# Performance work log

Measured on AMD Instinct MI355X. Metric: run time of the kernel, lower is better.

Reference implementation:

```python
import jax, jax.numpy as jnp
import numpy as np

D_MODEL = 512
STATE = 128
HALF = STATE // 2
SEQ = 4096
BATCH = 8


def setup_inputs() -> dict:
    key = jax.random.key(0)
    ks = jax.random.split(key, 4)
    u = jax.random.normal(ks[0], (BATCH, SEQ, D_MODEL), dtype=jnp.float32)
    # HiPPO init: Lambda = -0.5 + i*pi*n, n=1..HALF
    n = jnp.arange(1, HALF + 1, dtype=jnp.float32)
    log_Lambda_real = jnp.log(jnp.full((HALF,), 0.5, dtype=jnp.float32))  # log(-real) with real=-0.5
    Lambda_imag = jnp.pi * n
    B_real = jnp.ones((HALF, D_MODEL), dtype=jnp.float32)
    B_imag = jnp.zeros((HALF, D_MODEL), dtype=jnp.float32)
    C_real = jax.random.normal(ks[1], (D_MODEL, HALF), dtype=jnp.float32) / np.sqrt(STATE)
    C_imag = jax.random.normal(ks[2], (D_MODEL, HALF), dtype=jnp.float32) / np.sqrt(STATE)
    D = jax.random.normal(ks[3], (D_MODEL, D_MODEL), dtype=jnp.float32) / np.sqrt(D_MODEL)
    log_Delta = jnp.array([-3.0], dtype=jnp.float32)
    return {
        "u": u,
        "log_Lambda_real": log_Lambda_real,
        "Lambda_imag": Lambda_imag,
        "B_real": B_real,
        "B_imag": B_imag,
        "C_real": C_real,
        "C_imag": C_imag,
        "D": D,
        "log_Delta": log_Delta,
    }


def reference(u, log_Lambda_real, Lambda_imag, B_real, B_imag, C_real, C_imag, D, log_Delta):
    T = u.shape[1]
    Bc = B_real + 1j * B_imag            # (N/2, P) complex
    Cc = C_real + 1j * C_imag            # (P, N/2) complex
    # --- bilinear (Tustin) discretization ---
    Delta = jnp.exp(log_Delta)           # (1,)
    Lambda = -jnp.exp(jnp.clip(log_Lambda_real, -10.0, 10.0)) + 1j * Lambda_imag  # (N/2,)
    denom = 1.0 - (Delta / 2.0) * Lambda
    A_bar = (1.0 + (Delta / 2.0) * Lambda) / denom          # (N/2,)
    B_bar = (Delta / denom)[:, None] * Bc                   # (N/2, P)
    # --- FFT convolution with the SSM kernel k[n,t] = A_bar[n]^t ---
    t_idx = jnp.arange(T)
    k = jnp.exp(jnp.log(A_bar)[:, None] * t_idx[None, :])   # (N/2, T)
    u_c = u.astype(jnp.complex64)
    v = jnp.einsum('np,btp->bnt', B_bar, u_c)               # (B, N/2, T)
    fft_size = 2 * T
    V_f = jnp.fft.fft(v, n=fft_size, axis=-1)
    K_f = jnp.fft.fft(k, n=fft_size, axis=-1)
    conv = jnp.fft.ifft(V_f * K_f[None, :, :], axis=-1)[..., :T]  # (B, N/2, T)
    y = 2.0 * jnp.einsum('pn,bnt->btp', Cc, conv).real      # (B, T, P)
    return y + u @ D.T
```

## Files before the change

kernel.cpp:

```cpp
#include <hip/hip_runtime.h>
#include <hip/hip_bf16.h>
#include <stdint.h>


#define BATCH 8
#define SEQ   4096
#define DMODEL 512
#define HALF  64
#define CHUNK 64
#define NCHUNK (SEQ / CHUNK)
#define NT    10

typedef __attribute__((ext_vector_type(8))) short short8;
typedef __attribute__((ext_vector_type(4))) float f32x4;

__device__ __forceinline__ unsigned short f2bf(float f) {
    unsigned int u = __float_as_uint(f);
    u += 0x7fffu + ((u >> 16) & 1u);
    return (unsigned short)(u >> 16);
}
__device__ __forceinline__ float bf2f(unsigned short s) {
    return __uint_as_float((unsigned)s << 16);
}

__device__ __forceinline__ void poleA(const float* logLr, const float* Li_in,
                                      const float* logDelta, int n,
                                      float& Ar, float& Ai) {
    float Delta = expf(logDelta[0]);
    float llr = fminf(fmaxf(logLr[n], -10.f), 10.f);
    float Lr = -expf(llr);
    float Li = Li_in[n];
    float dr = 1.f - 0.5f * Delta * Lr;
    float di = -0.5f * Delta * Li;
    float dn = dr * dr + di * di;
    float nr = 1.f + 0.5f * Delta * Lr;
    float ni = 0.5f * Delta * Li;
    Ar = (nr * dr + ni * di) / dn;
    Ai = (ni * dr - nr * di) / dn;
}

__device__ __forceinline__ void cpow(float Ar, float Ai, int e,
                                     float& wr, float& wi) {
    wr = 1.f; wi = 0.f;
    float br = Ar, bi = Ai;
#pragma unroll
    for (int k = 0; k < 6; ++k) {
        if (e & 1) { float t = wr * br - wi * bi; wi = wr * bi + wi * br; wr = t; }
        float t2 = br * br - bi * bi; bi = 2.f * br * bi; br = t2;
        e >>= 1;
    }
}

#define GLOAD_LDS16(g, l)                                                    \
    __builtin_amdgcn_global_load_lds(                                        \
        (const __attribute__((address_space(1))) unsigned int*)(g),          \
        (__attribute__((address_space(3))) unsigned int*)(l), 16, 0, 0)

__global__ void k_build(const float* __restrict__ logLr, const float* __restrict__ Li_in,
                        const float* __restrict__ logDelta,
                        const float* __restrict__ Br, const float* __restrict__ Bi,
                        const float* __restrict__ Cr, const float* __restrict__ Ci,
                        const float* __restrict__ D,
                        unsigned short* __restrict__ Mv, unsigned short* __restrict__ W) {
    int bid = blockIdx.x;
    if (bid < 128) {
        int np = bid, p = threadIdx.x;
        if (p < DMODEL) {
            int n = np & 63;
            float Delta = expf(logDelta[0]);
            float llr = fminf(fmaxf(logLr[n], -10.f), 10.f);
            float Lr = -expf(llr);
            float Li = Li_in[n];
            float dr = 1.f - 0.5f * Delta * Lr;
            float di = -0.5f * Delta * Li;
            float dn = dr * dr + di * di;
            float sr = Delta * dr / dn;
            float si = -Delta * di / dn;
            float br = Br[n * DMODEL + p], bi = Bi[n * DMODEL + p];
            float v = (np < HALF) ? (sr * br - si * bi) : (si * br + sr * bi);
            Mv[np * DMODEL + p] = f2bf(v);
        }
    } else {
        int p = bid - 128, j = threadIdx.x;
        float v;
        if (j < HALF) v = 2.f * Cr[p * HALF + j];
        else if (j < 2 * HALF) v = -2.f * Ci[p * HALF + (j - HALF)];
        else v = D[p * DMODEL + (j - 2 * HALF)];
        W[p * 640 + j] = f2bf(v);
    }
}

__global__ void k_scanCB(const unsigned short* __restrict__ Vb,
                         const float* __restrict__ E,
                         const float* __restrict__ logLr, const float* __restrict__ Li_in,
                         const float* __restrict__ logDelta,
                         unsigned short* __restrict__ Xb) {
    int tid = threadIdx.x;
    int n = tid & 63;
    int c = ((blockIdx.x & 31) << 1) + (tid >> 6);
    int b = blockIdx.x >> 5;
    float Ar, Ai;
    poleA(logLr, Li_in, logDelta, n, Ar, Ai);
    float a64r = Ar, a64i = Ai;
#pragma unroll
    for (int s = 0; s < 6; ++s) {
        float t = a64r * a64r - a64i * a64i;
        a64i = 2.f * a64r * a64i;
        a64r = t;
    }
    float xr = 0.f, xi = 0.f, wr = 1.f, wi = 0.f;
    for (int jj = 1; jj <= c; ++jj) {
        int ei = ((b * NCHUNK + (c - jj)) * 2) * HALF + n;
        float er = E[ei], ev = E[ei + 64];
        xr += wr * er - wi * ev;
        xi += wr * ev + wi * er;
        float nwr = wr * a64r - wi * a64i;
        float nwi = wr * a64i + wi * a64r;
        wr = nwr; wi = nwi;
    }
    size_t base = ((size_t)b * SEQ + (size_t)c * CHUNK) * 128 + n;
    for (int tl = 0; tl < CHUNK; ++tl) {
        float vr = bf2f(Vb[base]), vi = bf2f(Vb[base + 64]);
        float nxr = Ar * xr - Ai * xi + vr;
        float nxi = Ar * xi + Ai * xr + vi;
        xr = nxr; xi = nxi;
        Xb[base] = f2bf(xr); Xb[base + 64] = f2bf(xi);
        base += 128;
    }
}

__global__ __launch_bounds__(512) void gemm1(const float* __restrict__ U,
                                             const unsigned short* __restrict__ Mv,
                                             unsigned short* __restrict__ Vb,
                                             unsigned short* __restrict__ Ub,
                                             const float* __restrict__ logLr,
                                             const float* __restrict__ Li_in,
                                             const float* __restrict__ logDelta,
                                             float* __restrict__ E) {
    __shared__ __align__(16) unsigned short As[64 * 32];
    __shared__ __align__(16) unsigned short Bs[128 * 32];
    __shared__ float Ered[8][2][16][2];
    const int tid = threadIdx.x;
    const int lane = tid & 63;
    const int w = tid >> 6;
    const int wm = w >> 2, wn = w & 3;
    const int l15 = lane & 15, l4 = lane >> 4;
    const int row0 = blockIdx.x * 64;
    const int srow = tid >> 3;
    const int sh = (tid & 7) * 4;

    f32x4 acc[2][2];
#pragma unroll
    for (int m = 0; m < 2; ++m)
#pragma unroll
        for (int n = 0; n < 2; ++n) acc[m][n] = (f32x4)(0.f);

    for (int k0 = 0; k0 < DMODEL; k0 += 32) {
        const float4 av = *(const float4*)(U + (size_t)(row0 + srow) * DMODEL + k0 + sh);

        __syncthreads();

        GLOAD_LDS16(Mv + (size_t)(tid >> 2) * DMODEL + k0 + (tid & 3) * 8,
                    &Bs[(w * 64) * 8]);

        uint2 wa;
        wa.x = (unsigned)f2bf(av.x) | ((unsigned)f2bf(av.y) << 16);
        wa.y = (unsigned)f2bf(av.z) | ((unsigned)f2bf(av.w) << 16);
        *(uint2*)&As[srow * 32 + sh] = wa;
        *(uint2*)&Ub[(size_t)(row0 + srow) * DMODEL + k0 + sh] = wa;

        __syncthreads();

        short8 af[2], bf[2];
#pragma unroll
        for (int m = 0; m < 2; ++m)
            af[m] = *(const short8*)&As[(wm * 32 + m * 16 + l15) * 32 + l4 * 8];
#pragma unroll
        for (int n = 0; n < 2; ++n)
            bf[n] = *(const short8*)&Bs[(wn * 32 + n * 16 + l15) * 32 + l4 * 8];
#pragma unroll
        for (int m = 0; m < 2; ++m)
#pragma unroll
            for (int n = 0; n < 2; ++n)
                acc[m][n] = __builtin_amdgcn_mfma_f32_16x16x32_bf16(af[m], bf[n], acc[m][n], 0, 0, 0);
    }

#pragma unroll
    for (int m = 0; m < 2; ++m) {
        int rbase = row0 + wm * 32 + m * 16 + l4 * 4;
#pragma unroll
        for (int n = 0; n < 2; ++n) {
            int col = wn * 32 + n * 16 + l15;
#pragma unroll
            for (int r = 0; r < 4; ++r)
                Vb[(size_t)(rbase + r) * 128 + col] = f2bf(acc[m][n][r]);
        }
    }

    {
        const int base = wm * 32 + l4 * 4;
        const int isIm = (wn >= 2);
#pragma unroll
        for (int nf = 0; nf < 2; ++nf) {
            int pole = ((wn & 1) * 32) + nf * 16 + l15;
            float Ar, Ai;
            poleA(logLr, Li_in, logDelta, pole, Ar, Ai);
            float a2r = Ar * Ar - Ai * Ai, a2i = 2.f * Ar * Ai;
            float a4r = a2r * a2r - a2i * a2i, a4i = 2.f * a2r * a2i;
            float a8r = a4r * a4r - a4i * a4i, a8i = 2.f * a4r * a4i;
            float a12r = a8r * a4r - a8i * a4i, a12i = a8r * a4i + a8i * a4r;
            float wr, wi;
            cpow(Ar, Ai, 44 - base, wr, wi);
            float s2re = 0.f, s2im = 0.f;
#pragma unroll
            for (int m = 1; m >= 0; --m) {
#pragma unroll
                for (int r = 3; r >= 0; --r) {
                    float v = acc[m][nf][r];
                    if (isIm) { s2re -= wi * v; s2im += wr * v; }
                    else      { s2re += wr * v; s2im += wi * v; }
                    float nwr = wr * Ar - wi * Ai;
                    float nwi = wr * Ai + wi * Ar;
                    wr = nwr; wi = nwi;
                }
                if (m == 1) {
                    float nwr = wr * a12r - wi * a12i;
                    float nwi = wr * a12i + wi * a12r;
                    wr = nwr; wi = nwi;
                }
            }
            s2re += __shfl_xor(s2re, 16, 64);
            s2re += __shfl_xor(s2re, 32, 64);
            s2im += __shfl_xor(s2im, 16, 64);
            s2im += __shfl_xor(s2im, 32, 64);
            if (l4 == 0) {
                Ered[w][nf][l15][0] = s2re;
                Ered[w][nf][l15][1] = s2im;
            }
        }
    }
    __syncthreads();
    if (tid < 128) {
        int p = tid & 63;
        int comp = tid >> 6;
        int wn1 = p >> 5;
        int nf = (p >> 4) & 1;
        int l = p & 15;
        float s = Ered[0 * 4 + wn1][nf][l][comp] + Ered[0 * 4 + wn1 + 2][nf][l][comp]
                + Ered[1 * 4 + wn1][nf][l][comp] + Ered[1 * 4 + wn1 + 2][nf][l][comp];
        int b = row0 >> 12;
        int c = (row0 >> 6) & 63;
        E[((b * NCHUNK + c) * 2) * HALF + comp * 64 + p] = s;
    }
}


#define STAGE_K(t, kh, j) do {                                                 \
    int c_ = (kh) * 1024 + (j) * 512 + tid;                                    \
    int ct_ = c_ ^ (((c_ >> 5) & 1) << 1);                                     \
    int r_ = (ct_ >> 2) & 255;                                                 \
    int kcol_ = (t) * 64 + (kh) * 32 + (ct_ & 3) * 8;                          \
    const unsigned short* asrc_ = (kcol_ < 128)                                \
        ? Xb + (size_t)(row0 + r_) * 128 + kcol_                               \
        : Ub + (size_t)(row0 + r_) * 512 + (kcol_ - 128);                      \
    GLOAD_LDS16(asrc_, &As[((t) & 1) * 16384 + ((kh) * 1024 + (j) * 512 + w * 64) * 8]); \
    GLOAD_LDS16(W + (size_t)(col0 + r_) * 640 + kcol_,                         \
                &Bs[((t) & 1) * 16384 + ((kh) * 1024 + (j) * 512 + w * 64) * 8]); \
} while (0)

#define LDAB(t, kh) do {                                                       \
    _Pragma("unroll") for (int i_ = 0; i_ < 8; ++i_) {                         \
        int r_ = wm * 128 + i_ * 16 + l15;                                     \
        int c_ = (l4 * 8) ^ (((r_ >> 3) & 1) << 4);                            \
        af[i_] = *(const short8*)&As[((t) & 1) * 16384 + (kh) * 8192 + r_ * 32 + c_]; \
    }                                                                          \
    _Pragma("unroll") for (int j_ = 0; j_ < 4; ++j_) {                         \
        int r_ = wn * 64 + j_ * 16 + l15;                                      \
        int c_ = (l4 * 8) ^ (((r_ >> 3) & 1) << 4);                            \
        bf[j_] = *(const short8*)&Bs[((t) & 1) * 16384 + (kh) * 8192 + r_ * 32 + c_]; \
    } } while (0)

#define MFMA32() do {                                                          \
    __builtin_amdgcn_s_setprio(1);                                             \
    _Pragma("unroll") for (int i_ = 0; i_ < 8; ++i_)                           \
    _Pragma("unroll") for (int j_ = 0; j_ < 4; ++j_)                           \
        acc[i_][j_] = __builtin_amdgcn_mfma_f32_16x16x32_bf16(                 \
            bf[j_], af[i_], acc[i_][j_], 0, 0, 0);                             \
    __builtin_amdgcn_s_setprio(0);                                             \
} while (0)

#define PHASE_SYNC(N) do {                                                     \
    asm volatile("s_waitcnt vmcnt(" #N ")" ::: "memory");                      \
    __builtin_amdgcn_s_barrier();                                              \
    __builtin_amdgcn_sched_barrier(0);                                         \
} while (0)

__global__ __launch_bounds__(512) void gemm23_8p(const unsigned short* __restrict__ Xb,
                                                 const unsigned short* __restrict__ Ub,
                                                 const unsigned short* __restrict__ W,
                                                 float* __restrict__ C) {
    __shared__ __align__(16) unsigned short As[2 * 16384];
    __shared__ __align__(16) unsigned short Bs[2 * 16384];
    const int tid = threadIdx.x;
    const int lane = tid & 63;
    const int w = tid >> 6;
    const int wm = w >> 2, wn = w & 3;
    const int l15 = lane & 15, l4 = lane >> 4;

    int lin = blockIdx.y * gridDim.x + blockIdx.x;
    int sw = (lin & 7) * 32 + (lin >> 3);
    const int row0 = (sw & 127) * 256;
    const int col0 = (sw >> 7) * 256;

    f32x4 acc[8][4];
#pragma unroll
    for (int m = 0; m < 8; ++m)
#pragma unroll
        for (int n = 0; n < 4; ++n) acc[m][n] = (f32x4)(0.f);

    STAGE_K(0, 0, 0); STAGE_K(0, 0, 1);
    STAGE_K(0, 1, 0); STAGE_K(0, 1, 1);
    STAGE_K(1, 0, 0); STAGE_K(1, 0, 1);

    short8 af[8], bf[4];
    for (int t = 0; t < NT - 1; ++t) {
        PHASE_SYNC(8);
        LDAB(t, 0);
        STAGE_K(t + 1, 1, 0); STAGE_K(t + 1, 1, 1);
        MFMA32();
        PHASE_SYNC(8);
        LDAB(t, 1);
        if (t < NT - 2) { STAGE_K(t + 2, 0, 0); STAGE_K(t + 2, 0, 1); }
        MFMA32();
    }
    PHASE_SYNC(4);
    LDAB(NT - 1, 0);
    MFMA32();
    PHASE_SYNC(0);
    LDAB(NT - 1, 1);
    MFMA32();

#pragma unroll
    for (int i = 0; i < 8; ++i) {
        int row = row0 + wm * 128 + i * 16 + l15;
#pragma unroll
        for (int j = 0; j < 4; ++j) {
            int col = col0 + wn * 64 + j * 16 + l4 * 4;
            *(float4*)&C[(size_t)row * DMODEL + col] =
                make_float4(acc[i][j][0], acc[i][j][1], acc[i][j][2], acc[i][j][3]);
        }
    }
}


extern "C" void kernel_launch(void* const* d_in, const int* in_sizes, int n_in,
                              void* d_out, int out_size, void* d_ws, size_t ws_size,
                              hipStream_t stream) {
    const float* u      = (const float*)d_in[0];
    const float* logLr  = (const float*)d_in[1];
    const float* Li     = (const float*)d_in[2];
    const float* Br     = (const float*)d_in[3];
    const float* Bi     = (const float*)d_in[4];
    const float* Cr     = (const float*)d_in[5];
    const float* Ci     = (const float*)d_in[6];
    const float* D      = (const float*)d_in[7];
    const float* logDel = (const float*)d_in[8];
    float* out = (float*)d_out;

    const size_t M = (size_t)BATCH * SEQ;
    unsigned short* Vb = (unsigned short*)d_ws;
    unsigned short* Ub = Vb + M * 128;
    unsigned short* Xb = Ub + M * 512;
    unsigned short* Mv = Xb + M * 128;
    unsigned short* W  = Mv + 128 * 512;
    float* E     = (float*)(W + 512 * 640);

    hipLaunchKernelGGL(k_build, dim3(640), dim3(640), 0, stream,
                       logLr, Li, logDel, Br, Bi, Cr, Ci, D, Mv, W);

    hipLaunchKernelGGL(gemm1, dim3(M / 64), dim3(512), 0, stream,
                       u, Mv, Vb, Ub, logLr, Li, logDel, E);

    hipLaunchKernelGGL(k_scanCB, dim3(256), dim3(128), 0, stream,
                       Vb, E, logLr, Li, logDel, Xb);

    hipLaunchKernelGGL(gemm23_8p, dim3(M / 256, DMODEL / 256), dim3(512), 0, stream,
                       Xb, Ub, W, out);
}
```

Measured before the change: 78.24 us.

## Replace LDS-staged pipelined GEMM with direct global-to-register operand loads

The final GEMM no longer stages A/B tiles through double-buffered shared memory with global-to-LDS loads and barriers. Each lane now loads its MFMA operand fragments straight from global memory into registers, split into a 128-wide X pass and a 512-wide U pass, and drops all barriers. This removes LDS traffic and synchronisation. The cost is that data shared across waves is no longer reused through LDS, so global and L2 loads grow, and there is no explicit prefetch to hide memory latency.

```diff
diff --git a/kernel.cpp b/kernel.cpp
--- a/kernel.cpp
+++ b/kernel.cpp
@@ -9,7 +9,6 @@
 #define HALF  64
 #define CHUNK 64
 #define NCHUNK (SEQ / CHUNK)
-#define NT    10
 
 typedef __attribute__((ext_vector_type(8))) short short8;
 typedef __attribute__((ext_vector_type(4))) float f32x4;
@@ -255,32 +254,7 @@
 }
 
 
-#define STAGE_K(t, kh, j) do {                                                 \
-    int c_ = (kh) * 1024 + (j) * 512 + tid;                                    \
-    int ct_ = c_ ^ (((c_ >> 5) & 1) << 1);                                     \
-    int r_ = (ct_ >> 2) & 255;                                                 \
-    int kcol_ = (t) * 64 + (kh) * 32 + (ct_ & 3) * 8;                          \
-    const unsigned short* asrc_ = (kcol_ < 128)                                \
-        ? Xb + (size_t)(row0 + r_) * 128 + kcol_                               \
-        : Ub + (size_t)(row0 + r_) * 512 + (kcol_ - 128);                      \
-    GLOAD_LDS16(asrc_, &As[((t) & 1) * 16384 + ((kh) * 1024 + (j) * 512 + w * 64) * 8]); \
-    GLOAD_LDS16(W + (size_t)(col0 + r_) * 640 + kcol_,                         \
-                &Bs[((t) & 1) * 16384 + ((kh) * 1024 + (j) * 512 + w * 64) * 8]); \
-} while (0)
-
-#define LDAB(t, kh) do {                                                       \
-    _Pragma("unroll") for (int i_ = 0; i_ < 8; ++i_) {                         \
-        int r_ = wm * 128 + i_ * 16 + l15;                                     \
-        int c_ = (l4 * 8) ^ (((r_ >> 3) & 1) << 4);                            \
-        af[i_] = *(const short8*)&As[((t) & 1) * 16384 + (kh) * 8192 + r_ * 32 + c_]; \
-    }                                                                          \
-    _Pragma("unroll") for (int j_ = 0; j_ < 4; ++j_) {                         \
-        int r_ = wn * 64 + j_ * 16 + l15;                                      \
-        int c_ = (l4 * 8) ^ (((r_ >> 3) & 1) << 4);                            \
-        bf[j_] = *(const short8*)&Bs[((t) & 1) * 16384 + (kh) * 8192 + r_ * 32 + c_]; \
-    } } while (0)
-
-#define MFMA32() do {                                                          \
+#define MFMA32R() do {                                                         \
     __builtin_amdgcn_s_setprio(1);                                             \
     _Pragma("unroll") for (int i_ = 0; i_ < 8; ++i_)                           \
     _Pragma("unroll") for (int j_ = 0; j_ < 4; ++j_)                           \
@@ -289,18 +263,10 @@
     __builtin_amdgcn_s_setprio(0);                                             \
 } while (0)
 
-#define PHASE_SYNC(N) do {                                                     \
-    asm volatile("s_waitcnt vmcnt(" #N ")" ::: "memory");                      \
-    __builtin_amdgcn_s_barrier();                                              \
-    __builtin_amdgcn_sched_barrier(0);                                         \
-} while (0)
-
-__global__ __launch_bounds__(512) void gemm23_8p(const unsigned short* __restrict__ Xb,
-                                                 const unsigned short* __restrict__ Ub,
-                                                 const unsigned short* __restrict__ W,
-                                                 float* __restrict__ C) {
-    __shared__ __align__(16) unsigned short As[2 * 16384];
-    __shared__ __align__(16) unsigned short Bs[2 * 16384];
+__global__ __launch_bounds__(512) void gemm23_reg(const unsigned short* __restrict__ Xb,
+                                                  const unsigned short* __restrict__ Ub,
+                                                  const unsigned short* __restrict__ W,
+                                                  float* __restrict__ C) {
     const int tid = threadIdx.x;
     const int lane = tid & 63;
     const int w = tid >> 6;
@@ -318,27 +284,35 @@
 #pragma unroll
         for (int n = 0; n < 4; ++n) acc[m][n] = (f32x4)(0.f);
 
-    STAGE_K(0, 0, 0); STAGE_K(0, 0, 1);
-    STAGE_K(0, 1, 0); STAGE_K(0, 1, 1);
-    STAGE_K(1, 0, 0); STAGE_K(1, 0, 1);
+    const unsigned short* aX = Xb + (size_t)(row0 + wm * 128 + l15) * 128 + l4 * 8;
+    const unsigned short* aU = Ub + (size_t)(row0 + wm * 128 + l15) * 512 + l4 * 8;
+    const unsigned short* bW = W + (size_t)(col0 + wn * 64 + l15) * 640 + l4 * 8;
 
     short8 af[8], bf[4];
-    for (int t = 0; t < NT - 1; ++t) {
-        PHASE_SYNC(8);
-        LDAB(t, 0);
-        STAGE_K(t + 1, 1, 0); STAGE_K(t + 1, 1, 1);
-        MFMA32();
-        PHASE_SYNC(8);
-        LDAB(t, 1);
-        if (t < NT - 2) { STAGE_K(t + 2, 0, 0); STAGE_K(t + 2, 0, 1); }
-        MFMA32();
-    }
-    PHASE_SYNC(4);
-    LDAB(NT - 1, 0);
-    MFMA32();
-    PHASE_SYNC(0);
-    LDAB(NT - 1, 1);
-    MFMA32();
+
+#pragma unroll
+    for (int p = 0; p < 4; ++p) {
+        const int kcol = p * 32;
+#pragma unroll
+        for (int i = 0; i < 8; ++i)
+            af[i] = *(const short8*)(aX + i * (16 * 128) + kcol);
+#pragma unroll
+        for (int j = 0; j < 4; ++j)
+            bf[j] = *(const short8*)(bW + j * (16 * 640) + kcol);
+        MFMA32R();
+    }
+
+#pragma unroll 4
+    for (int p = 0; p < 16; ++p) {
+        const int kcol = p * 32;
+#pragma unroll
+        for (int i = 0; i < 8; ++i)
+            af[i] = *(const short8*)(aU + i * (16 * 512) + kcol);
+#pragma unroll
+        for (int j = 0; j < 4; ++j)
+            bf[j] = *(const short8*)(bW + j * (16 * 640) + 128 + kcol);
+        MFMA32R();
+    }
 
 #pragma unroll
     for (int i = 0; i < 8; ++i) {
@@ -384,6 +358,6 @@
     hipLaunchKernelGGL(k_scanCB, dim3(256), dim3(128), 0, stream,
                        Vb, E, logLr, Li, logDel, Xb);
 
-    hipLaunchKernelGGL(gemm23_8p, dim3(M / 256, DMODEL / 256), dim3(512), 0, stream,
+    hipLaunchKernelGGL(gemm23_reg, dim3(M / 256, DMODEL / 256), dim3(512), 0, stream,
                        Xb, Ub, W, out);
 }
```

Measured after the change: 111.2 us. 1.42x slower.
